# Optimization experiments

Measured on AMD Instinct MI355X. Metric: run time of the kernel, lower is better.

## Reference

```python
import jax, jax.numpy as jnp
import numpy as np

B, T, C, H = 2, 2048, 1024, 16
HD = C // H  # 64


def setup_inputs() -> dict:
    key = jax.random.key(0)
    ks = jax.random.split(key, 5)
    x = jax.random.normal(ks[0], (B, T, C), jnp.float32)
    scale = 0.02
    Wq = jax.random.normal(ks[1], (C, C), jnp.float32) * scale
    Wk = jax.random.normal(ks[2], (C, C), jnp.float32) * scale
    Wv = jax.random.normal(ks[3], (C, C), jnp.float32) * scale
    Wo = jax.random.normal(ks[4], (C, C), jnp.float32) * scale
    # RoPE tables: freqs_cis = exp(i * pos * theta_j), theta_j = 10000^(-2j/HD)
    pos = jnp.arange(T, dtype=jnp.float32)
    theta = 10000.0 ** (-jnp.arange(0, HD, 2, dtype=jnp.float32) / HD)  # [HD/2]
    ang = pos[:, None] * theta[None, :]  # [T, HD/2]
    cos = jnp.cos(ang)
    sin = jnp.sin(ang)
    return {"x": x, "Wq": Wq, "Wk": Wk, "Wv": Wv, "Wo": Wo, "cos": cos, "sin": sin}


def _rope(t, cos, sin):
    # t: [B,T,H,HD]; pairs (even, odd) along last dim form complex numbers
    b, s, h, hd = t.shape
    tr = t.reshape(b, s, h, hd // 2, 2)
    t0, t1 = tr[..., 0], tr[..., 1]
    c = cos[None, :, None, :]  # [1,T,1,HD/2]
    sn = sin[None, :, None, :]
    o0 = t0 * c - t1 * sn
    o1 = t0 * sn + t1 * c
    return jnp.stack([o0, o1], axis=-1).reshape(b, s, h, hd)


def reference(x, Wq, Wk, Wv, Wo, cos, sin):
    b, t, c = x.shape
    h, hd = H, c // H
    q = (x @ Wq.T).reshape(b, t, h, hd)
    k = (x @ Wk.T).reshape(b, t, h, hd)
    v = (x @ Wv.T).reshape(b, t, h, hd)
    q = _rope(q, cos, sin)
    k = _rope(k, cos, sin)
    # explicit causal attention with full TxT score matrix (as in source)
    att = jnp.einsum("bthd,bshd->bhts", q, k) / jnp.sqrt(jnp.float32(hd))
    causal = jnp.tril(jnp.ones((t, t), dtype=bool))
    att = jnp.where(causal[None, None, :, :], att, -jnp.inf)
    att = jax.nn.softmax(att, axis=-1)
    out = jnp.einsum("bhts,bshd->bthd", att, v).reshape(b, t, c)
    return out @ Wo.T
```

## Files before the change

kernel.cpp:

```cpp
#include <hip/hip_runtime.h>
#include <cstdint>
#include <cstddef>


typedef __bf16 bf16;
typedef float  f32x4  __attribute__((ext_vector_type(4)));
typedef float  f32x16 __attribute__((ext_vector_type(16)));
typedef __bf16 bf16x4 __attribute__((ext_vector_type(4)));
typedef __bf16 bf16x8 __attribute__((ext_vector_type(8)));

constexpr int Bb = 2, Tt = 2048, Cc = 1024, Hh = 16;
constexpr int Mrows = Bb * Tt;
constexpr int NT = Tt / 64;
constexpr int LDS_ = 72;

#define GLOAD_LDS16(gp, lp)                                                      \
    __builtin_amdgcn_global_load_lds(                                            \
        (const __attribute__((address_space(1))) void*)(gp),                     \
        (__attribute__((address_space(3))) void*)(lp), 16, 0, 0)

#define QUAD_T(v0, v1, v2, v3, c2)                                               \
    {                                                                            \
        float e0 = (c2 & 1) ? v0 : v1, e1 = (c2 & 1) ? v2 : v3;                  \
        e0 = __shfl_xor(e0, 1); e1 = __shfl_xor(e1, 1);                          \
        if (c2 & 1) { v0 = e0; v2 = e1; } else { v1 = e0; v3 = e1; }             \
        float f0 = (c2 & 2) ? v0 : v2, f1 = (c2 & 2) ? v1 : v3;                  \
        f0 = __shfl_xor(f0, 2); f1 = __shfl_xor(f1, 2);                          \
        if (c2 & 2) { v0 = f0; v1 = f1; } else { v2 = f0; v3 = f1; }             \
    }

__device__ inline unsigned pkb(float a, float b)
{
    unsigned r;
    asm("v_cvt_pk_bf16_f32 %0, %1, %2" : "=v"(r) : "v"(a), "v"(b));
    return r;
}

__global__ __launch_bounds__(256) void convert_k(const float* __restrict__ x,
                                                 const float* __restrict__ Wq,
                                                 const float* __restrict__ Wk,
                                                 const float* __restrict__ Wv,
                                                 const float* __restrict__ Wo,
                                                 const float* __restrict__ cosb,
                                                 const float* __restrict__ sinb,
                                                 bf16* __restrict__ xb,
                                                 bf16* __restrict__ Wqkv,
                                                 bf16* __restrict__ Wob,
                                                 float2* __restrict__ cs)
{
    if (blockIdx.x >= 4096) {
        int pi = ((blockIdx.x - 4096) * 256 + threadIdx.x) * 8;
#pragma unroll
        for (int u = 0; u < 8; ++u)
            cs[pi + u] = float2{cosb[pi + u], sinb[pi + u]};
        return;
    }
    uint32_t id = blockIdx.x * 256 + threadIdx.x;
    const float* src; bf16* dst; float sc = 1.0f;
    if (id < 524288u) {
        uint32_t tile = id >> 10, slot = id & 1023;
        uint32_t row = (tile >> 4) * 128 + (slot >> 9) * 64 +
                       ((slot >> 6) & 3) * 16 + (slot & 15);
        uint32_t k = (tile & 15) * 64 + ((slot >> 8) & 1) * 32 + ((slot >> 4) & 3) * 8;
        src = x + (size_t)row * 1024 + k;
        dst = xb + (size_t)id * 8;
    } else if (id < 917504u) {
        uint32_t t2 = id - 524288u;
        uint32_t tile = t2 >> 10, slot = t2 & 1023;
        uint32_t n = (tile >> 4) * 128 + (slot >> 9) * 64 +
                     ((slot >> 6) & 3) * 16 + (slot & 15);
        uint32_t k = (tile & 15) * 64 + ((slot >> 8) & 1) * 32 + ((slot >> 4) & 3) * 8;
        if (n < 1024)      { src = Wq + (size_t)n * 1024 + k;
                             sc = 0.125f * 1.44269504088896f; }
        else if (n < 2048)   src = Wk + (size_t)(n - 1024) * 1024 + k;
        else                 src = Wv + (size_t)(n - 2048) * 1024 + k;
        dst = Wqkv + (size_t)t2 * 8;
    } else {
        uint32_t t3 = id - 917504u;
        uint32_t tile = t3 >> 9, slot = t3 & 511;
        uint32_t n = (tile >> 4) * 64 + (slot >> 8) * 32 +
                     ((slot >> 6) & 1) * 16 + (slot & 15);
        uint32_t k = (tile & 15) * 64 + ((slot >> 7) & 1) * 32 + ((slot >> 4) & 3) * 8;
        src = Wo + (size_t)n * 1024 + k;
        dst = Wob + (size_t)t3 * 8;
    }
    float4 v0 = *(const float4*)(src);
    float4 v1 = *(const float4*)(src + 4);
    bf16x8 t;
    t[0] = (bf16)(v0.x*sc); t[1] = (bf16)(v0.y*sc); t[2] = (bf16)(v0.z*sc); t[3] = (bf16)(v0.w*sc);
    t[4] = (bf16)(v1.x*sc); t[5] = (bf16)(v1.y*sc); t[6] = (bf16)(v1.z*sc); t[7] = (bf16)(v1.w*sc);
    *(bf16x8*)dst = t;
}

__global__ __launch_bounds__(256) void gemm_qkv(const bf16* __restrict__ A,
                                                const bf16* __restrict__ W,
                                                bf16* __restrict__ QK,
                                                bf16* __restrict__ Vt,
                                                const float2* __restrict__ cs)
{
    __shared__ bf16 As[8192];
    __shared__ bf16 Ws[8192];
    const int tid  = threadIdx.x;
    const int lane = tid & 63, wave = tid >> 6;
    const int rhw = wave >> 1, chw = wave & 1;
    const int wr = rhw * 64, wc = chw * 64;
    const int l16 = lane & 15, lq = lane >> 4;
    const int row0 = blockIdx.x * 128, col0 = blockIdx.y * 128;

    f32x4 acc[4][4];
#pragma unroll
    for (int i = 0; i < 4; ++i)
#pragma unroll
        for (int j = 0; j < 4; ++j) acc[i][j] = f32x4{0.f, 0.f, 0.f, 0.f};

    const bf16* At = A + (size_t)blockIdx.x * 16 * 8192;
    const bf16* Wt = W + (size_t)blockIdx.y * 16 * 8192;

    for (int kb = 0; kb < 16; ++kb) {
        const bf16* at = At + kb * 8192;
        const bf16* wt = Wt + kb * 8192;
#pragma unroll
        for (int rnd = 0; rnd < 4; ++rnd) {
            const int seg = rnd * 4 + wave;
            GLOAD_LDS16(at + seg * 512 + lane * 8, &As[seg * 512]);
            GLOAD_LDS16(wt + seg * 512 + lane * 8, &Ws[seg * 512]);
        }
        __syncthreads();
#pragma unroll
        for (int ks = 0; ks < 2; ++ks) {
            bf16x8 af[4], bfr[4];
#pragma unroll
            for (int i = 0; i < 4; ++i)
                af[i] = *(const bf16x8*)(&As[(rhw * 512 + ks * 256 + i * 64 + lq * 16 + l16) * 8]);
#pragma unroll
            for (int j = 0; j < 4; ++j)
                bfr[j] = *(const bf16x8*)(&Ws[(chw * 512 + ks * 256 + j * 64 + lq * 16 + l16) * 8]);
#pragma unroll
            for (int i = 0; i < 4; ++i)
#pragma unroll
                for (int j = 0; j < 4; ++j)
                    acc[i][j] = __builtin_amdgcn_mfma_f32_16x16x32_bf16(
                        af[i], bfr[j], acc[i][j], 0, 0, 0);
        }
        __syncthreads();
    }

    const int c2 = l16 & 3, g4 = (l16 >> 2) * 4;
    if (blockIdx.y < 16) {
#pragma unroll
        for (int i = 0; i < 4; ++i)
#pragma unroll
            for (int j = 0; j < 4; ++j) {
                float v0 = acc[i][j][0], v1 = acc[i][j][1];
                float v2 = acc[i][j][2], v3 = acc[i][j][3];
                QUAD_T(v0, v1, v2, v3, c2);
                const int row = row0 + wr + i * 16 + lq * 4 + c2;
                const int t   = row & (Tt - 1);
                const int colb = wc + j * 16 + g4;
                const int p0   = (colb & 63) >> 1;
                float4 cp = *(const float4*)(&cs[t * 32 + p0]);
                bf16x4 pk;
                pk[0] = (bf16)(v0 * cp.x - v1 * cp.y);
                pk[1] = (bf16)(v0 * cp.y + v1 * cp.x);
                pk[2] = (bf16)(v2 * cp.z - v3 * cp.w);
                pk[3] = (bf16)(v2 * cp.w + v3 * cp.z);
                *(bf16x4*)(&QK[(size_t)row * 2048 + col0 + colb]) = pk;
            }
    } else {
#pragma unroll
        for (int i = 0; i < 4; ++i)
#pragma unroll
            for (int j = 0; j < 4; ++j) {
                const int dfull = col0 - 2048 + wc + j * 16 + l16;
                const int h = dfull >> 6, d = dfull & 63;
                const int row = row0 + wr + i * 16 + lq * 4;
                const int b = row >> 11, t = row & (Tt - 1);
                bf16x4 pk;
                pk[0] = (bf16)acc[i][j][0]; pk[1] = (bf16)acc[i][j][1];
                pk[2] = (bf16)acc[i][j][2]; pk[3] = (bf16)acc[i][j][3];
                *(bf16x4*)(&Vt[((size_t)(b * 16 + h) * 64 + d) * (size_t)Tt + t]) = pk;
            }
    }
}

__global__ __launch_bounds__(256) void gemm_o(const bf16* __restrict__ A,
                                              const bf16* __restrict__ W,
                                              float* __restrict__ Out)
{
    __shared__ bf16 As[8192];
    __shared__ bf16 Ws[4096];
    const int tid  = threadIdx.x;
    const int lane = tid & 63, wave = tid >> 6;
    const int rhw = wave >> 1, chw = wave & 1;
    const int wr = rhw * 64, wc = chw * 32;
    const int l16 = lane & 15, lq = lane >> 4;
    const int row0 = blockIdx.x * 128, col0 = blockIdx.y * 64;

    f32x4 acc[4][2];
#pragma unroll
    for (int i = 0; i < 4; ++i)
#pragma unroll
        for (int j = 0; j < 2; ++j) acc[i][j] = f32x4{0.f, 0.f, 0.f, 0.f};

    const bf16* At = A + (size_t)blockIdx.x * 16 * 8192;
    const bf16* Wt = W + (size_t)blockIdx.y * 16 * 4096;

    for (int kb = 0; kb < 16; ++kb) {
        const bf16* at = At + kb * 8192;
        const bf16* wt = Wt + kb * 4096;
#pragma unroll
        for (int rnd = 0; rnd < 4; ++rnd) {
            const int seg = rnd * 4 + wave;
            GLOAD_LDS16(at + seg * 512 + lane * 8, &As[seg * 512]);
        }
#pragma unroll
        for (int rnd = 0; rnd < 2; ++rnd) {
            const int seg = rnd * 4 + wave;
            GLOAD_LDS16(wt + seg * 512 + lane * 8, &Ws[seg * 512]);
        }
        __syncthreads();
#pragma unroll
        for (int ks = 0; ks < 2; ++ks) {
            bf16x8 af[4], bfr[2];
#pragma unroll
            for (int i = 0; i < 4; ++i)
                af[i] = *(const bf16x8*)(&As[(rhw * 512 + ks * 256 + i * 64 + lq * 16 + l16) * 8]);
#pragma unroll
            for (int j = 0; j < 2; ++j)
                bfr[j] = *(const bf16x8*)(&Ws[(chw * 256 + ks * 128 + j * 64 + lq * 16 + l16) * 8]);
#pragma unroll
            for (int i = 0; i < 4; ++i)
#pragma unroll
                for (int j = 0; j < 2; ++j)
                    acc[i][j] = __builtin_amdgcn_mfma_f32_16x16x32_bf16(
                        af[i], bfr[j], acc[i][j], 0, 0, 0);
        }
        __syncthreads();
    }
    const int c2 = l16 & 3, g4 = (l16 >> 2) * 4;
#pragma unroll
    for (int i = 0; i < 4; ++i)
#pragma unroll
        for (int j = 0; j < 2; ++j) {
            float v0 = acc[i][j][0], v1 = acc[i][j][1];
            float v2 = acc[i][j][2], v3 = acc[i][j][3];
            QUAD_T(v0, v1, v2, v3, c2);
            const int row = row0 + wr + i * 16 + lq * 4 + c2;
            const int col = col0 + wc + j * 16 + g4;
            *(float4*)(&Out[(size_t)row * Cc + col]) = float4{v0, v1, v2, v3};
        }
}

__global__ __launch_bounds__(128, 2) void attn_k(const bf16* __restrict__ QK,
                                                 const bf16* __restrict__ Vt,
                                                 bf16* __restrict__ O)
{
    __shared__ bf16 Ks[2][64 * LDS_];
    __shared__ bf16 Vs[2][64 * LDS_];
    const int tid = threadIdx.x;
    const int wv = tid >> 6, lane = tid & 63;
    const int l31 = lane & 31, hf = lane >> 5;
    const int id = blockIdx.y * gridDim.x + blockIdx.x;
    const int bh = (id & 7) * 4 + ((id >> 3) & 3);
    const int s8 = (id >> 5) & 7, rnd4 = id >> 8;
    const int qt = (rnd4 == 0) ? 31 - s8 : (rnd4 == 1) ? 16 + s8
                 : (rnd4 == 2) ? 15 - s8 : s8;
    const int b = bh >> 4, h = bh & 15;
    const int kr = tid >> 1, c0 = (tid & 1) * 32;

    const bf16* kcol = QK + 1024 + (size_t)(b * Tt + kr) * 2048 + h * 64 + c0;
    const bf16* vcol = Vt + ((size_t)bh * 64 + kr) * Tt + c0;

    const int qglob = qt * 64 + wv * 32 + l31;
    const bf16* qp = QK + (size_t)(b * Tt + qglob) * 2048 + h * 64 + hf * 8;
    const bf16x8 qf0 = *(const bf16x8*)(qp);
    const bf16x8 qf1 = *(const bf16x8*)(qp + 16);
    const bf16x8 qf2 = *(const bf16x8*)(qp + 32);
    const bf16x8 qf3 = *(const bf16x8*)(qp + 48);

    uint4 ka0 = *(const uint4*)(kcol);
    uint4 ka1 = *(const uint4*)(kcol + 8);
    uint4 ka2 = *(const uint4*)(kcol + 16);
    uint4 ka3 = *(const uint4*)(kcol + 24);
    uint4 va0 = *(const uint4*)(vcol);
    uint4 va1 = *(const uint4*)(vcol + 8);
    uint4 va2 = *(const uint4*)(vcol + 16);
    uint4 va3 = *(const uint4*)(vcol + 24);
    {
        bf16* kd = &Ks[0][kr * LDS_ + c0];
        bf16* vd = &Vs[0][kr * LDS_ + c0];
        *(uint4*)(kd)      = ka0; *(uint4*)(kd + 8)  = ka1;
        *(uint4*)(kd + 16) = ka2; *(uint4*)(kd + 24) = ka3;
        *(uint4*)(vd)      = va0; *(uint4*)(vd + 8)  = va1;
        *(uint4*)(vd + 16) = va2; *(uint4*)(vd + 24) = va3;
    }
    __syncthreads();

    float la = 0.f, lb = 0.f, lc = 0.f, ld = 0.f;
    f32x16 o0, o1;
#pragma unroll
    for (int r = 0; r < 16; ++r) { o0[r] = 0.f; o1[r] = 0.f; }

    for (int t = 0; t <= qt; ++t) {
        const int cur = t & 1;
        if (t < qt) {
            const bf16* kn = kcol + (size_t)(t + 1) * 64 * 2048;
            const bf16* vn = vcol + (t + 1) * 64;
            ka0 = *(const uint4*)(kn);      ka1 = *(const uint4*)(kn + 8);
            ka2 = *(const uint4*)(kn + 16); ka3 = *(const uint4*)(kn + 24);
            va0 = *(const uint4*)(vn);      va1 = *(const uint4*)(vn + 8);
            va2 = *(const uint4*)(vn + 16); va3 = *(const uint4*)(vn + 24);
        }

        f32x16 s0, s1;
#pragma unroll
        for (int r = 0; r < 16; ++r) { s0[r] = 0.f; s1[r] = 0.f; }
        {
            const bf16* kb0 = &Ks[cur][l31 * LDS_ + hf * 8];
            const bf16* kb1 = &Ks[cur][(32 + l31) * LDS_ + hf * 8];
            bf16x8 a;
            a = *(const bf16x8*)(kb0);      s0 = __builtin_amdgcn_mfma_f32_32x32x16_bf16(a, qf0, s0, 0, 0, 0);
            a = *(const bf16x8*)(kb0 + 16); s0 = __builtin_amdgcn_mfma_f32_32x32x16_bf16(a, qf1, s0, 0, 0, 0);
            a = *(const bf16x8*)(kb0 + 32); s0 = __builtin_amdgcn_mfma_f32_32x32x16_bf16(a, qf2, s0, 0, 0, 0);
            a = *(const bf16x8*)(kb0 + 48); s0 = __builtin_amdgcn_mfma_f32_32x32x16_bf16(a, qf3, s0, 0, 0, 0);
            a = *(const bf16x8*)(kb1);      s1 = __builtin_amdgcn_mfma_f32_32x32x16_bf16(a, qf0, s1, 0, 0, 0);
            a = *(const bf16x8*)(kb1 + 16); s1 = __builtin_amdgcn_mfma_f32_32x32x16_bf16(a, qf1, s1, 0, 0, 0);
            a = *(const bf16x8*)(kb1 + 32); s1 = __builtin_amdgcn_mfma_f32_32x32x16_bf16(a, qf2, s1, 0, 0, 0);
            a = *(const bf16x8*)(kb1 + 48); s1 = __builtin_amdgcn_mfma_f32_32x32x16_bf16(a, qf3, s1, 0, 0, 0);
        }
        if (t == qt) {
            const int kbase = t * 64 + 4 * hf;
#pragma unroll
            for (int r = 0; r < 16; ++r) {
                const int key0 = kbase + (r & 3) + 8 * (r >> 2);
                if (key0 > qglob)      s0[r] = -1e30f;
                if (key0 + 32 > qglob) s1[r] = -1e30f;
            }
        }
#pragma unroll
        for (int r = 0; r < 16; ++r) {
            s0[r] = exp2f(s0[r]);
            s1[r] = exp2f(s1[r]);
            if (r & 1) { lb += s0[r]; ld += s1[r]; }
            else       { la += s0[r]; lc += s1[r]; }
        }
        bf16x8 pb0, pb1, pb2, pb3;
        {
            unsigned X, Y, Z, W;
            union { unsigned u[4]; bf16x8 h; } tmp;
            X = pkb(s0[0],  s0[1]);  Y = pkb(s0[2],  s0[3]);
            Z = pkb(s0[4],  s0[5]);  W = pkb(s0[6],  s0[7]);
            asm("v_permlane32_swap_b32 %0, %1" : "+v"(X), "+v"(Z));
            asm("v_permlane32_swap_b32 %0, %1" : "+v"(Y), "+v"(W));
            tmp.u[0] = X; tmp.u[1] = Y; tmp.u[2] = Z; tmp.u[3] = W; pb0 = tmp.h;
            X = pkb(s0[8],  s0[9]);  Y = pkb(s0[10], s0[11]);
            Z = pkb(s0[12], s0[13]); W = pkb(s0[14], s0[15]);
            asm("v_permlane32_swap_b32 %0, %1" : "+v"(X), "+v"(Z));
            asm("v_permlane32_swap_b32 %0, %1" : "+v"(Y), "+v"(W));
            tmp.u[0] = X; tmp.u[1] = Y; tmp.u[2] = Z; tmp.u[3] = W; pb1 = tmp.h;
            X = pkb(s1[0],  s1[1]);  Y = pkb(s1[2],  s1[3]);
            Z = pkb(s1[4],  s1[5]);  W = pkb(s1[6],  s1[7]);
            asm("v_permlane32_swap_b32 %0, %1" : "+v"(X), "+v"(Z));
            asm("v_permlane32_swap_b32 %0, %1" : "+v"(Y), "+v"(W));
            tmp.u[0] = X; tmp.u[1] = Y; tmp.u[2] = Z; tmp.u[3] = W; pb2 = tmp.h;
            X = pkb(s1[8],  s1[9]);  Y = pkb(s1[10], s1[11]);
            Z = pkb(s1[12], s1[13]); W = pkb(s1[14], s1[15]);
            asm("v_permlane32_swap_b32 %0, %1" : "+v"(X), "+v"(Z));
            asm("v_permlane32_swap_b32 %0, %1" : "+v"(Y), "+v"(W));
            tmp.u[0] = X; tmp.u[1] = Y; tmp.u[2] = Z; tmp.u[3] = W; pb3 = tmp.h;
        }
        {
            const bf16* vb0 = &Vs[cur][l31 * LDS_ + hf * 8];
            const bf16* vb1 = &Vs[cur][(32 + l31) * LDS_ + hf * 8];
            bf16x8 v;
            v = *(const bf16x8*)(vb0);      o0 = __builtin_amdgcn_mfma_f32_32x32x16_bf16(v, pb0, o0, 0, 0, 0);
            v = *(const bf16x8*)(vb0 + 16); o0 = __builtin_amdgcn_mfma_f32_32x32x16_bf16(v, pb1, o0, 0, 0, 0);
            v = *(const bf16x8*)(vb0 + 32); o0 = __builtin_amdgcn_mfma_f32_32x32x16_bf16(v, pb2, o0, 0, 0, 0);
            v = *(const bf16x8*)(vb0 + 48); o0 = __builtin_amdgcn_mfma_f32_32x32x16_bf16(v, pb3, o0, 0, 0, 0);
            v = *(const bf16x8*)(vb1);      o1 = __builtin_amdgcn_mfma_f32_32x32x16_bf16(v, pb0, o1, 0, 0, 0);
            v = *(const bf16x8*)(vb1 + 16); o1 = __builtin_amdgcn_mfma_f32_32x32x16_bf16(v, pb1, o1, 0, 0, 0);
            v = *(const bf16x8*)(vb1 + 32); o1 = __builtin_amdgcn_mfma_f32_32x32x16_bf16(v, pb2, o1, 0, 0, 0);
            v = *(const bf16x8*)(vb1 + 48); o1 = __builtin_amdgcn_mfma_f32_32x32x16_bf16(v, pb3, o1, 0, 0, 0);
        }
        if (t < qt) {
            bf16* kd = &Ks[cur ^ 1][kr * LDS_ + c0];
            bf16* vd = &Vs[cur ^ 1][kr * LDS_ + c0];
            *(uint4*)(kd)      = ka0; *(uint4*)(kd + 8)  = ka1;
            *(uint4*)(kd + 16) = ka2; *(uint4*)(kd + 24) = ka3;
            *(uint4*)(vd)      = va0; *(uint4*)(vd + 8)  = va1;
            *(uint4*)(vd + 16) = va2; *(uint4*)(vd + 24) = va3;
        }
        __syncthreads();
    }
    float lsum = (la + lb) + (lc + ld);
    lsum += __shfl_xor(lsum, 32);
    const float inv = 1.f / lsum;

    bf16* obase = O + ((size_t)(16 * b + (qt >> 1)) * 16 + h) * 8192;
    const int rh = qt & 1;
    const int slot_row = (lane & 15) | (((2 * wv + ((lane >> 4) & 1)) & 3) << 6) |
                         (rh << 9);
#pragma unroll
    for (int g = 0; g < 4; ++g) {
        bf16x4 w0, w1;
#pragma unroll
        for (int r = 0; r < 4; ++r) {
            w0[r] = (bf16)(o0[4 * g + r] * inv);
            w1[r] = (bf16)(o1[4 * g + r] * inv);
        }
        *(bf16x4*)(obase + (slot_row | (g << 4)) * 8 + 4 * hf) = w0;
        *(bf16x4*)(obase + (slot_row | (g << 4) | 256) * 8 + 4 * hf) = w1;
    }
}

extern "C" void kernel_launch(void* const* d_in, const int* in_sizes, int n_in,
                              void* d_out, int out_size, void* d_ws, size_t ws_size,
                              hipStream_t stream)
{
    const float* x    = (const float*)d_in[0];
    const float* Wq   = (const float*)d_in[1];
    const float* Wk   = (const float*)d_in[2];
    const float* Wv   = (const float*)d_in[3];
    const float* Wo   = (const float*)d_in[4];
    const float* cosb = (const float*)d_in[5];
    const float* sinb = (const float*)d_in[6];

    constexpr size_t M1 = 1024 * 1024;
    bf16* base = (bf16*)d_ws;
    bf16*   xb   = base;
    bf16*   QK   = base + 4 * M1;
    bf16*   VtG  = base + 12 * M1;
    bf16*   Wqkv = base + 16 * M1;
    bf16*   Wob  = base + 19 * M1;
    float2* csT  = (float2*)(base + 20 * M1);
    bf16*   Ow   = xb;

    convert_k<<<4096 + 32, 256, 0, stream>>>(x, Wq, Wk, Wv, Wo, cosb, sinb,
                                             xb, Wqkv, Wob, csT);

    gemm_qkv<<<dim3(Mrows / 128, 3072 / 128), 256, 0, stream>>>(
        xb, Wqkv, QK, VtG, csT);

    attn_k<<<dim3(32, 32), 128, 0, stream>>>(QK, VtG, Ow);

    gemm_o<<<dim3(Mrows / 128, Cc / 64), 256, 0, stream>>>(Ow, Wob, (float*)d_out);
}
```

Before: 185.3 us.

## Split attention key tile across four waves with LDS reduction of partial outputs

The attention block grows from 2 to 4 waves. Each query half is now handled by two waves that each process 32 of the 64 keys per tile, and the per-wave work per tile is halved. Partial O accumulators and row sums are merged through LDS scratch at the end before normalisation. The aim is more waves in flight to hide MFMA and exp latency, at the cost of an extra LDS reduction and barrier, and higher register and occupancy demands from the new launch bounds.

```diff
diff --git a/kernel.cpp b/kernel.cpp
--- a/kernel.cpp
+++ b/kernel.cpp
@@ -251,7 +251,7 @@
         }
 }
 
-__global__ __launch_bounds__(128, 2) void attn_k(const bf16* __restrict__ QK,
+__global__ __launch_bounds__(256, 4) void attn_k(const bf16* __restrict__ QK,
                                                  const bf16* __restrict__ Vt,
                                                  bf16* __restrict__ O)
 {
@@ -260,18 +260,19 @@
     const int tid = threadIdx.x;
     const int wv = tid >> 6, lane = tid & 63;
     const int l31 = lane & 31, hf = lane >> 5;
+    const int qh = wv & 1, kh = wv >> 1;
     const int id = blockIdx.y * gridDim.x + blockIdx.x;
     const int bh = (id & 7) * 4 + ((id >> 3) & 3);
     const int s8 = (id >> 5) & 7, rnd4 = id >> 8;
     const int qt = (rnd4 == 0) ? 31 - s8 : (rnd4 == 1) ? 16 + s8
                  : (rnd4 == 2) ? 15 - s8 : s8;
     const int b = bh >> 4, h = bh & 15;
-    const int kr = tid >> 1, c0 = (tid & 1) * 32;
+    const int kr = tid >> 2, c0 = (tid & 3) * 16;
 
     const bf16* kcol = QK + 1024 + (size_t)(b * Tt + kr) * 2048 + h * 64 + c0;
     const bf16* vcol = Vt + ((size_t)bh * 64 + kr) * Tt + c0;
 
-    const int qglob = qt * 64 + wv * 32 + l31;
+    const int qglob = qt * 64 + qh * 32 + l31;
     const bf16* qp = QK + (size_t)(b * Tt + qglob) * 2048 + h * 64 + hf * 8;
     const bf16x8 qf0 = *(const bf16x8*)(qp);
     const bf16x8 qf1 = *(const bf16x8*)(qp + 16);
@@ -280,23 +281,17 @@
 
     uint4 ka0 = *(const uint4*)(kcol);
     uint4 ka1 = *(const uint4*)(kcol + 8);
-    uint4 ka2 = *(const uint4*)(kcol + 16);
-    uint4 ka3 = *(const uint4*)(kcol + 24);
     uint4 va0 = *(const uint4*)(vcol);
     uint4 va1 = *(const uint4*)(vcol + 8);
-    uint4 va2 = *(const uint4*)(vcol + 16);
-    uint4 va3 = *(const uint4*)(vcol + 24);
     {
         bf16* kd = &Ks[0][kr * LDS_ + c0];
         bf16* vd = &Vs[0][kr * LDS_ + c0];
-        *(uint4*)(kd)      = ka0; *(uint4*)(kd + 8)  = ka1;
-        *(uint4*)(kd + 16) = ka2; *(uint4*)(kd + 24) = ka3;
-        *(uint4*)(vd)      = va0; *(uint4*)(vd + 8)  = va1;
-        *(uint4*)(vd + 16) = va2; *(uint4*)(vd + 24) = va3;
+        *(uint4*)(kd)     = ka0; *(uint4*)(kd + 8) = ka1;
+        *(uint4*)(vd)     = va0; *(uint4*)(vd + 8) = va1;
     }
     __syncthreads();
 
-    float la = 0.f, lb = 0.f, lc = 0.f, ld = 0.f;
+    float la = 0.f, lb = 0.f;
     f32x16 o0, o1;
 #pragma unroll
     for (int r = 0; r < 16; ++r) { o0[r] = 0.f; o1[r] = 0.f; }
@@ -306,110 +301,108 @@
         if (t < qt) {
             const bf16* kn = kcol + (size_t)(t + 1) * 64 * 2048;
             const bf16* vn = vcol + (t + 1) * 64;
-            ka0 = *(const uint4*)(kn);      ka1 = *(const uint4*)(kn + 8);
-            ka2 = *(const uint4*)(kn + 16); ka3 = *(const uint4*)(kn + 24);
-            va0 = *(const uint4*)(vn);      va1 = *(const uint4*)(vn + 8);
-            va2 = *(const uint4*)(vn + 16); va3 = *(const uint4*)(vn + 24);
-        }
-
-        f32x16 s0, s1;
-#pragma unroll
-        for (int r = 0; r < 16; ++r) { s0[r] = 0.f; s1[r] = 0.f; }
+            ka0 = *(const uint4*)(kn); ka1 = *(const uint4*)(kn + 8);
+            va0 = *(const uint4*)(vn); va1 = *(const uint4*)(vn + 8);
+        }
+
+        f32x16 s;
+#pragma unroll
+        for (int r = 0; r < 16; ++r) s[r] = 0.f;
         {
-            const bf16* kb0 = &Ks[cur][l31 * LDS_ + hf * 8];
-            const bf16* kb1 = &Ks[cur][(32 + l31) * LDS_ + hf * 8];
+            const bf16* kb = &Ks[cur][(kh * 32 + l31) * LDS_ + hf * 8];
             bf16x8 a;
-            a = *(const bf16x8*)(kb0);      s0 = __builtin_amdgcn_mfma_f32_32x32x16_bf16(a, qf0, s0, 0, 0, 0);
-            a = *(const bf16x8*)(kb0 + 16); s0 = __builtin_amdgcn_mfma_f32_32x32x16_bf16(a, qf1, s0, 0, 0, 0);
-            a = *(const bf16x8*)(kb0 + 32); s0 = __builtin_amdgcn_mfma_f32_32x32x16_bf16(a, qf2, s0, 0, 0, 0);
-            a = *(const bf16x8*)(kb0 + 48); s0 = __builtin_amdgcn_mfma_f32_32x32x16_bf16(a, qf3, s0, 0, 0, 0);
-            a = *(const bf16x8*)(kb1);      s1 = __builtin_amdgcn_mfma_f32_32x32x16_bf16(a, qf0, s1, 0, 0, 0);
-            a = *(const bf16x8*)(kb1 + 16); s1 = __builtin_amdgcn_mfma_f32_32x32x16_bf16(a, qf1, s1, 0, 0, 0);
-            a = *(const bf16x8*)(kb1 + 32); s1 = __builtin_amdgcn_mfma_f32_32x32x16_bf16(a, qf2, s1, 0, 0, 0);
-            a = *(const bf16x8*)(kb1 + 48); s1 = __builtin_amdgcn_mfma_f32_32x32x16_bf16(a, qf3, s1, 0, 0, 0);
+            a = *(const bf16x8*)(kb);      s = __builtin_amdgcn_mfma_f32_32x32x16_bf16(a, qf0, s, 0, 0, 0);
+            a = *(const bf16x8*)(kb + 16); s = __builtin_amdgcn_mfma_f32_32x32x16_bf16(a, qf1, s, 0, 0, 0);
+            a = *(const bf16x8*)(kb + 32); s = __builtin_amdgcn_mfma_f32_32x32x16_bf16(a, qf2, s, 0, 0, 0);
+            a = *(const bf16x8*)(kb + 48); s = __builtin_amdgcn_mfma_f32_32x32x16_bf16(a, qf3, s, 0, 0, 0);
         }
         if (t == qt) {
-            const int kbase = t * 64 + 4 * hf;
+            const int kbase = t * 64 + kh * 32 + 4 * hf;
 #pragma unroll
             for (int r = 0; r < 16; ++r) {
                 const int key0 = kbase + (r & 3) + 8 * (r >> 2);
-                if (key0 > qglob)      s0[r] = -1e30f;
-                if (key0 + 32 > qglob) s1[r] = -1e30f;
+                if (key0 > qglob) s[r] = -1e30f;
             }
         }
 #pragma unroll
         for (int r = 0; r < 16; ++r) {
-            s0[r] = exp2f(s0[r]);
-            s1[r] = exp2f(s1[r]);
-            if (r & 1) { lb += s0[r]; ld += s1[r]; }
-            else       { la += s0[r]; lc += s1[r]; }
-        }
-        bf16x8 pb0, pb1, pb2, pb3;
+            s[r] = exp2f(s[r]);
+            if (r & 1) lb += s[r]; else la += s[r];
+        }
+        bf16x8 pb0, pb1;
         {
             unsigned X, Y, Z, W;
             union { unsigned u[4]; bf16x8 h; } tmp;
-            X = pkb(s0[0],  s0[1]);  Y = pkb(s0[2],  s0[3]);
-            Z = pkb(s0[4],  s0[5]);  W = pkb(s0[6],  s0[7]);
+            X = pkb(s[0],  s[1]);  Y = pkb(s[2],  s[3]);
+            Z = pkb(s[4],  s[5]);  W = pkb(s[6],  s[7]);
             asm("v_permlane32_swap_b32 %0, %1" : "+v"(X), "+v"(Z));
             asm("v_permlane32_swap_b32 %0, %1" : "+v"(Y), "+v"(W));
             tmp.u[0] = X; tmp.u[1] = Y; tmp.u[2] = Z; tmp.u[3] = W; pb0 = tmp.h;
-            X = pkb(s0[8],  s0[9]);  Y = pkb(s0[10], s0[11]);
-            Z = pkb(s0[12], s0[13]); W = pkb(s0[14], s0[15]);
+            X = pkb(s[8],  s[9]);  Y = pkb(s[10], s[11]);
+            Z = pkb(s[12], s[13]); W = pkb(s[14], s[15]);
             asm("v_permlane32_swap_b32 %0, %1" : "+v"(X), "+v"(Z));
             asm("v_permlane32_swap_b32 %0, %1" : "+v"(Y), "+v"(W));
             tmp.u[0] = X; tmp.u[1] = Y; tmp.u[2] = Z; tmp.u[3] = W; pb1 = tmp.h;
-            X = pkb(s1[0],  s1[1]);  Y = pkb(s1[2],  s1[3]);
-            Z = pkb(s1[4],  s1[5]);  W = pkb(s1[6],  s1[7]);
-            asm("v_permlane32_swap_b32 %0, %1" : "+v"(X), "+v"(Z));
-            asm("v_permlane32_swap_b32 %0, %1" : "+v"(Y), "+v"(W));
-            tmp.u[0] = X; tmp.u[1] = Y; tmp.u[2] = Z; tmp.u[3] = W; pb2 = tmp.h;
-            X = pkb(s1[8],  s1[9]);  Y = pkb(s1[10], s1[11]);
-            Z = pkb(s1[12], s1[13]); W = pkb(s1[14], s1[15]);
-            asm("v_permlane32_swap_b32 %0, %1" : "+v"(X), "+v"(Z));
-            asm("v_permlane32_swap_b32 %0, %1" : "+v"(Y), "+v"(W));
-            tmp.u[0] = X; tmp.u[1] = Y; tmp.u[2] = Z; tmp.u[3] = W; pb3 = tmp.h;
         }
         {
-            const bf16* vb0 = &Vs[cur][l31 * LDS_ + hf * 8];
-            const bf16* vb1 = &Vs[cur][(32 + l31) * LDS_ + hf * 8];
+            const bf16* vb0 = &Vs[cur][l31 * LDS_ + kh * 32 + hf * 8];
+            const bf16* vb1 = &Vs[cur][(32 + l31) * LDS_ + kh * 32 + hf * 8];
             bf16x8 v;
             v = *(const bf16x8*)(vb0);      o0 = __builtin_amdgcn_mfma_f32_32x32x16_bf16(v, pb0, o0, 0, 0, 0);
             v = *(const bf16x8*)(vb0 + 16); o0 = __builtin_amdgcn_mfma_f32_32x32x16_bf16(v, pb1, o0, 0, 0, 0);
-            v = *(const bf16x8*)(vb0 + 32); o0 = __builtin_amdgcn_mfma_f32_32x32x16_bf16(v, pb2, o0, 0, 0, 0);
-            v = *(const bf16x8*)(vb0 + 48); o0 = __builtin_amdgcn_mfma_f32_32x32x16_bf16(v, pb3, o0, 0, 0, 0);
             v = *(const bf16x8*)(vb1);      o1 = __builtin_amdgcn_mfma_f32_32x32x16_bf16(v, pb0, o1, 0, 0, 0);
             v = *(const bf16x8*)(vb1 + 16); o1 = __builtin_amdgcn_mfma_f32_32x32x16_bf16(v, pb1, o1, 0, 0, 0);
-            v = *(const bf16x8*)(vb1 + 32); o1 = __builtin_amdgcn_mfma_f32_32x32x16_bf16(v, pb2, o1, 0, 0, 0);
-            v = *(const bf16x8*)(vb1 + 48); o1 = __builtin_amdgcn_mfma_f32_32x32x16_bf16(v, pb3, o1, 0, 0, 0);
         }
         if (t < qt) {
             bf16* kd = &Ks[cur ^ 1][kr * LDS_ + c0];
             bf16* vd = &Vs[cur ^ 1][kr * LDS_ + c0];
-            *(uint4*)(kd)      = ka0; *(uint4*)(kd + 8)  = ka1;
-            *(uint4*)(kd + 16) = ka2; *(uint4*)(kd + 24) = ka3;
-            *(uint4*)(vd)      = va0; *(uint4*)(vd + 8)  = va1;
-            *(uint4*)(vd + 16) = va2; *(uint4*)(vd + 24) = va3;
+            *(uint4*)(kd)     = ka0; *(uint4*)(kd + 8) = ka1;
+            *(uint4*)(vd)     = va0; *(uint4*)(vd + 8) = va1;
         }
         __syncthreads();
     }
-    float lsum = (la + lb) + (lc + ld);
+    float lsum = la + lb;
     lsum += __shfl_xor(lsum, 32);
-    const float inv = 1.f / lsum;
-
-    bf16* obase = O + ((size_t)(16 * b + (qt >> 1)) * 16 + h) * 8192;
-    const int rh = qt & 1;
-    const int slot_row = (lane & 15) | (((2 * wv + ((lane >> 4) & 1)) & 3) << 6) |
-                         (rh << 9);
-#pragma unroll
-    for (int g = 0; g < 4; ++g) {
-        bf16x4 w0, w1;
-#pragma unroll
-        for (int r = 0; r < 4; ++r) {
-            w0[r] = (bf16)(o0[4 * g + r] * inv);
-            w1[r] = (bf16)(o1[4 * g + r] * inv);
-        }
-        *(bf16x4*)(obase + (slot_row | (g << 4)) * 8 + 4 * hf) = w0;
-        *(bf16x4*)(obase + (slot_row | (g << 4) | 256) * 8 + 4 * hf) = w1;
+
+    float* fscr = (float*)(&Ks[0][0]);
+    float* lscr = (float*)(&Vs[0][0]);
+    if (kh == 1) {
+        float* sb = fscr + qh * (64 * 33);
+#pragma unroll
+        for (int r = 0; r < 16; ++r) {
+            const int d = (r & 3) + 8 * (r >> 2) + 4 * hf;
+            sb[d * 33 + l31]        = o0[r];
+            sb[(d + 32) * 33 + l31] = o1[r];
+        }
+        if (hf == 0) lscr[qh * 32 + l31] = lsum;
+    }
+    __syncthreads();
+    if (kh == 0) {
+        const float* sb = fscr + qh * (64 * 33);
+#pragma unroll
+        for (int r = 0; r < 16; ++r) {
+            const int d = (r & 3) + 8 * (r >> 2) + 4 * hf;
+            o0[r] += sb[d * 33 + l31];
+            o1[r] += sb[(d + 32) * 33 + l31];
+        }
+        lsum += lscr[qh * 32 + l31];
+        const float inv = 1.f / lsum;
+
+        bf16* obase = O + ((size_t)(16 * b + (qt >> 1)) * 16 + h) * 8192;
+        const int rh = qt & 1;
+        const int slot_row = (lane & 15) | (((2 * qh + ((lane >> 4) & 1)) & 3) << 6) |
+                             (rh << 9);
+#pragma unroll
+        for (int g = 0; g < 4; ++g) {
+            bf16x4 w0, w1;
+#pragma unroll
+            for (int r = 0; r < 4; ++r) {
+                w0[r] = (bf16)(o0[4 * g + r] * inv);
+                w1[r] = (bf16)(o1[4 * g + r] * inv);
+            }
+            *(bf16x4*)(obase + (slot_row | (g << 4)) * 8 + 4 * hf) = w0;
+            *(bf16x4*)(obase + (slot_row | (g << 4) | 256) * 8 + 4 * hf) = w1;
+        }
     }
 }
 
@@ -441,7 +434,7 @@
     gemm_qkv<<<dim3(Mrows / 128, 3072 / 128), 256, 0, stream>>>(
         xb, Wqkv, QK, VtG, csT);
 
-    attn_k<<<dim3(32, 32), 128, 0, stream>>>(QK, VtG, Ow);
+    attn_k<<<dim3(32, 32), 256, 0, stream>>>(QK, VtG, Ow);
 
     gemm_o<<<dim3(Mrows / 128, Cc / 64), 256, 0, stream>>>(Ow, Wob, (float*)d_out);
 }
```

Result: faster. 166.5 us (-10.1%).
